# Kernel tuning notes

Hardware: AMD Instinct MI355X
Metric: run time of the kernel (lower is better)

## Reference

```python
import jax, jax.numpy as jnp
import numpy as np

H = 1024      # hidden_size
L = 2         # num_layers
B = 4096      # batch_size (acts as sequential time axis)
IN = 33       # LSTM input size (17 raw + 8 ip-embed + 8 port-embed)


def setup_inputs() -> dict:
    key = jax.random.key(0)
    ks = jax.random.split(key, 16)
    s = 0.02
    return {
        "x": jax.random.normal(ks[0], (B, 17), dtype=jnp.float32),
        "ip": jax.random.randint(ks[1], (B, 8), 0, 256),
        "port": jax.random.randint(ks[2], (B, 2), 0, 70000),
        "hidden": jnp.zeros((L, 1, H), dtype=jnp.float32),
        "cell": jnp.zeros((L, 1, H), dtype=jnp.float32),
        "ip_emb": jax.random.normal(ks[3], (256, 1), dtype=jnp.float32) * s,
        "port_emb": jax.random.normal(ks[4], (70000, 4), dtype=jnp.float32) * s,
        "W_ih0": jax.random.normal(ks[5], (4 * H, IN), dtype=jnp.float32) * s,
        "W_hh0": jax.random.normal(ks[6], (4 * H, H), dtype=jnp.float32) * s,
        "b_ih0": jax.random.normal(ks[7], (4 * H,), dtype=jnp.float32) * s,
        "b_hh0": jax.random.normal(ks[8], (4 * H,), dtype=jnp.float32) * s,
        "W_ih1": jax.random.normal(ks[9], (4 * H, H), dtype=jnp.float32) * s,
        "W_hh1": jax.random.normal(ks[10], (4 * H, H), dtype=jnp.float32) * s,
        "b_ih1": jax.random.normal(ks[11], (4 * H,), dtype=jnp.float32) * s,
        "b_hh1": jax.random.normal(ks[12], (4 * H,), dtype=jnp.float32) * s,
    }


def reference(x, ip, port, hidden, cell, ip_emb, port_emb,
              W_ih0, W_hh0, b_ih0, b_hh0, W_ih1, W_hh1, b_ih1, b_hh1):
    # embedding lookups + concat -> [B, 33]
    ip_e = ip_emb[ip].reshape(B, -1)        # [B, 8]
    port_e = port_emb[port].reshape(B, -1)  # [B, 8]
    xin = jnp.concatenate((x, ip_e, port_e), axis=1)  # [B, 33]

    Wih = (W_ih0, W_ih1)
    Whh = (W_hh0, W_hh1)
    bih = (b_ih0, b_ih1)
    bhh = (b_hh0, b_hh1)

    h0 = hidden[:, 0]  # [L, H]
    c0 = cell[:, 0]    # [L, H]

    def step(carry, xt):
        h, c = carry
        inp = xt
        hs, cs = [], []
        for l in range(L):  # fixed small layer loop
            gates = Wih[l] @ inp + bih[l] + Whh[l] @ h[l] + bhh[l]  # [4H]
            i, f, g, o = jnp.split(gates, 4)  # PyTorch gate order: i,f,g,o
            i = jax.nn.sigmoid(i)
            f = jax.nn.sigmoid(f)
            g = jnp.tanh(g)
            o = jax.nn.sigmoid(o)
            c_new = f * c[l] + i * g
            h_new = o * jnp.tanh(c_new)
            hs.append(h_new)
            cs.append(c_new)
            inp = h_new
        return (jnp.stack(hs), jnp.stack(cs)), jax.nn.relu(inp)

    (hf, cf), outputs = jax.lax.scan(step, (h0, c0), xin)
    return outputs, (hf[:, None, :], cf[:, None, :])
```

## Files before the change

kernel.cpp:

```cpp
#include <hip/hip_runtime.h>
#include <hip/hip_fp16.h>
#include <math.h>

#define Hn 1024
#define Bn 4096
#define INW 33
#define OUTS (Bn * Hn)
#define TPB 512
#define ROWP 1024

typedef _Float16 half2v __attribute__((ext_vector_type(2)));
typedef unsigned uint4v __attribute__((ext_vector_type(4)));

__device__ __forceinline__ float sigmoidf_(float x) {
    return 1.0f / (1.0f + __expf(-x));
}
__device__ __forceinline__ float tanhf_(float x) {
    float e = __expf(-2.0f * fabsf(x));
    float r = (1.0f - e) / (1.0f + e);
    return copysignf(r, x);
}
__device__ __forceinline__ unsigned pack2(float a, float b) {
    __half2 h = __floats2half2_rn(a, b);
    return __builtin_bit_cast(unsigned, h);
}
__device__ __forceinline__ float dot2acc(unsigned w, unsigned hv, float acc) {
#if __has_builtin(__builtin_amdgcn_fdot2)
    return __builtin_amdgcn_fdot2(__builtin_bit_cast(half2v, w),
                                  __builtin_bit_cast(half2v, hv), acc, false);
#else
    __half2 wh = __builtin_bit_cast(__half2, w);
    __half2 hh = __builtin_bit_cast(__half2, hv);
    float2 wf = __half22float2(wh), hf = __half22float2(hh);
    return acc + wf.x * hf.x + wf.y * hf.y;
#endif
}

__device__ __forceinline__ unsigned spin_slice(const unsigned long long* slice,
                                               int lane, unsigned tag) {
    unsigned long long v;
    int rounds = 0;
    for (;;) {
        asm volatile("global_load_dwordx2 %0, %1, off sc0 sc1\n\t"
                     "s_waitcnt vmcnt(0)"
                     : "=v"(v) : "v"(slice + lane) : "memory");
        if (__all((unsigned)(v >> 32) == tag)) break;
        if (++rounds > (1 << 24)) break;
    }
    return (unsigned)v;
}

__device__ __forceinline__ void spin_slice2(const unsigned long long* sliceA,
                                            const unsigned long long* sliceB,
                                            int lane, unsigned tag,
                                            unsigned& dA, unsigned& dB) {
    unsigned long long va, vb;
    int rounds = 0;
    for (;;) {
        asm volatile("global_load_dwordx2 %0, %2, off sc0 sc1\n\t"
                     "global_load_dwordx2 %1, %3, off sc0 sc1\n\t"
                     "s_waitcnt vmcnt(0)"
                     : "=v"(va), "=v"(vb)
                     : "v"(sliceA + lane), "v"(sliceB + lane) : "memory");
        bool ok = ((unsigned)(va >> 32) == tag) & ((unsigned)(vb >> 32) == tag);
        if (__all(ok)) break;
        if (++rounds > (1 << 24)) break;
    }
    dA = (unsigned)va;
    dB = (unsigned)vb;
}

__device__ __forceinline__ void store16_coherent(void* dst, uint4v v) {
    asm volatile("global_store_dwordx4 %0, %1, off sc0 sc1"
                 :: "v"(dst), "v"(v) : "memory");
}

__global__ void prep_kernel(const float* __restrict__ x, const int* __restrict__ ip,
                            const int* __restrict__ port, const float* __restrict__ ip_emb,
                            const float* __restrict__ port_emb, float* __restrict__ xin) {
    int gid = blockIdx.x * blockDim.x + threadIdx.x;
    if (gid < Bn * INW) {
        int t = gid / INW;
        int k = gid - t * INW;
        float v;
        if (k < 17) {
            v = x[t * 17 + k];
        } else if (k < 25) {
            v = ip_emb[ip[t * 8 + (k - 17)]];
        } else {
            int kk = k - 25;
            v = port_emb[port[t * 2 + (kk >> 2)] * 4 + (kk & 3)];
        }
        xin[gid] = v;
    }
}

__global__ void __launch_bounds__(TPB, 2) lstm_kernel(
    const float* __restrict__ xin,
    const float* __restrict__ hid0, const float* __restrict__ cel0,
    const float* __restrict__ Wih0, const float* __restrict__ Whh0,
    const float* __restrict__ bih0, const float* __restrict__ bhh0,
    const float* __restrict__ Wih1, const float* __restrict__ Whh1,
    const float* __restrict__ bih1, const float* __restrict__ bhh1,
    float* __restrict__ out,
    unsigned long long* __restrict__ rowpkt)
{
    __shared__ unsigned hs2[2][1024];
    __shared__ unsigned long long stg[16];
    const int tid  = threadIdx.x;
    const int lane = tid & 63;
    const int wave = tid >> 6;
    const int bx   = blockIdx.x;

    if (bx < 32) {
        const int j0 = bx * 32 + wave * 4;
        unsigned w2[4][4][8];
        float    wx[4][4];
        float    bs[4][4];
#pragma unroll
        for (int jj = 0; jj < 4; ++jj) {
#pragma unroll
            for (int g = 0; g < 4; ++g) {
                const int row = g * Hn + (j0 + jj);
                const float* wr = Whh0 + (size_t)row * Hn;
#pragma unroll
                for (int k = 0; k < 8; ++k) {
                    int c = lane + 64 * k;
                    w2[jj][g][k] = pack2(wr[2 * c], wr[2 * c + 1]);
                }
                wx[jj][g] = (lane < INW) ? Wih0[row * INW + lane] : 0.0f;
                bs[jj][g] = bih0[row] + bhh0[row];
            }
        }
        float cst[4], hcur[4];
#pragma unroll
        for (int jj = 0; jj < 4; ++jj) { cst[jj] = cel0[j0 + jj]; hcur[jj] = 0.0f; }

        for (int s = 0; s < Bn; ++s) {
            const int b = s & 1;
            float xv = xin[s * INW + (lane < INW ? lane : 0)];
            if (s == 0) {
                int q = wave * 64 + lane;
                hs2[0][q] = pack2(hid0[2 * q], hid0[2 * q + 1]);
            } else {
                unsigned d = spin_slice(rowpkt + (size_t)(s - 1) * ROWP + wave * 64,
                                        lane, (unsigned)s);
                hs2[b][wave * 64 + lane] = d;
            }
            __syncthreads();

            float acc[4][4];
#pragma unroll
            for (int jj = 0; jj < 4; ++jj)
#pragma unroll
                for (int g = 0; g < 4; ++g) acc[jj][g] = wx[jj][g] * xv;
#pragma unroll
            for (int k = 0; k < 8; ++k) {
                unsigned hv = hs2[b][lane + 64 * k];
#pragma unroll
                for (int jj = 0; jj < 4; ++jj)
#pragma unroll
                    for (int g = 0; g < 4; ++g)
                        acc[jj][g] = dot2acc(w2[jj][g][k], hv, acc[jj][g]);
            }

#pragma unroll
            for (int off = 32; off >= 1; off >>= 1)
#pragma unroll
                for (int jj = 0; jj < 4; ++jj)
#pragma unroll
                    for (int g = 0; g < 4; ++g)
                        acc[jj][g] += __shfl_xor(acc[jj][g], off);

#pragma unroll
            for (int jj = 0; jj < 4; ++jj) {
                float gi = sigmoidf_(acc[jj][0] + bs[jj][0]);
                float gf = sigmoidf_(acc[jj][1] + bs[jj][1]);
                float gg = tanhf_   (acc[jj][2] + bs[jj][2]);
                float go = sigmoidf_(acc[jj][3] + bs[jj][3]);
                cst[jj] = gf * cst[jj] + gi * gg;
                hcur[jj] = go * tanhf_(cst[jj]);
            }
            if (lane == 0) {
                unsigned long long tw = ((unsigned long long)(s + 1)) << 32;
                stg[2 * wave]     = tw | pack2(hcur[0], hcur[1]);
                stg[2 * wave + 1] = tw | pack2(hcur[2], hcur[3]);
            }
            __syncthreads();
            if (wave == 0 && lane < 8) {
                uint4v v = *(const uint4v*)&stg[2 * lane];
                char* dst = (char*)(rowpkt + (size_t)s * ROWP) + bx * 128 + lane * 16;
                store16_coherent(dst, v);
            }
        }
        if (lane == 0) {
#pragma unroll
            for (int jj = 0; jj < 4; ++jj) {
                out[OUTS + j0 + jj] = hcur[jj];
                out[OUTS + 2 * Hn + j0 + jj] = cst[jj];
            }
        }
    } else {
        const int blk = bx - 32;
        const int j0  = blk * 16 + wave * 2;
        unsigned w2[2][4][16];
        float    bs[2][4];
#pragma unroll
        for (int jj = 0; jj < 2; ++jj) {
#pragma unroll
            for (int g = 0; g < 4; ++g) {
                const int row = g * Hn + (j0 + jj);
                const float* wr1 = Wih1 + (size_t)row * Hn;
                const float* wr2 = Whh1 + (size_t)row * Hn;
#pragma unroll
                for (int k = 0; k < 8; ++k) {
                    int c = lane + 64 * k;
                    w2[jj][g][k]     = pack2(wr1[2 * c], wr1[2 * c + 1]);
                    w2[jj][g][8 + k] = pack2(wr2[2 * c], wr2[2 * c + 1]);
                }
                bs[jj][g] = bih1[row] + bhh1[row];
            }
        }
        float cst[2], hcur[2];
#pragma unroll
        for (int jj = 0; jj < 2; ++jj) { cst[jj] = cel0[Hn + j0 + jj]; hcur[jj] = 0.0f; }

        if (wave == 0 && lane < 4) {
            int base = Hn + blk * 16 + 4 * lane;
            uint4v v;
            v.x = pack2(hid0[base],     hid0[base + 1]);  v.y = 1u;
            v.z = pack2(hid0[base + 2], hid0[base + 3]);  v.w = 1u;
            char* dst = (char*)(rowpkt + 512) + blk * 64 + lane * 16;
            store16_coherent(dst, v);
        }

        for (int s = 1; s <= Bn; ++s) {
            const int t = s - 1;
            const int b = s & 1;
            const unsigned long long* rb = rowpkt + (size_t)(s - 1) * ROWP;
            unsigned dA, dB;
            spin_slice2(rb + wave * 64, rb + 512 + wave * 64, lane, (unsigned)s, dA, dB);
            hs2[b][wave * 64 + lane]       = dA;
            hs2[b][512 + wave * 64 + lane] = dB;
            __syncthreads();

            float acc[2][4];
#pragma unroll
            for (int jj = 0; jj < 2; ++jj)
#pragma unroll
                for (int g = 0; g < 4; ++g) acc[jj][g] = 0.0f;
#pragma unroll
            for (int k = 0; k < 16; ++k) {
                unsigned hv = hs2[b][lane + 64 * k];
#pragma unroll
                for (int jj = 0; jj < 2; ++jj)
#pragma unroll
                    for (int g = 0; g < 4; ++g)
                        acc[jj][g] = dot2acc(w2[jj][g][k], hv, acc[jj][g]);
            }

#pragma unroll
            for (int off = 32; off >= 1; off >>= 1)
#pragma unroll
                for (int jj = 0; jj < 2; ++jj)
#pragma unroll
                    for (int g = 0; g < 4; ++g)
                        acc[jj][g] += __shfl_xor(acc[jj][g], off);

#pragma unroll
            for (int jj = 0; jj < 2; ++jj) {
                float gi = sigmoidf_(acc[jj][0] + bs[jj][0]);
                float gf = sigmoidf_(acc[jj][1] + bs[jj][1]);
                float gg = tanhf_   (acc[jj][2] + bs[jj][2]);
                float go = sigmoidf_(acc[jj][3] + bs[jj][3]);
                cst[jj] = gf * cst[jj] + gi * gg;
                hcur[jj] = go * tanhf_(cst[jj]);
            }
            if (lane == 0) {
                unsigned long long tw = ((unsigned long long)(s + 1)) << 32;
                stg[wave] = tw | pack2(hcur[0], hcur[1]);
                float2 o2 = make_float2(fmaxf(hcur[0], 0.0f), fmaxf(hcur[1], 0.0f));
                *(float2*)(out + (size_t)t * Hn + j0) = o2;
            }
            __syncthreads();
            if (wave == 0 && lane < 4) {
                uint4v v = *(const uint4v*)&stg[2 * lane];
                char* dst = (char*)(rowpkt + (size_t)s * ROWP + 512) + blk * 64 + lane * 16;
                store16_coherent(dst, v);
            }
        }
        if (lane == 0) {
#pragma unroll
            for (int jj = 0; jj < 2; ++jj) {
                out[OUTS + Hn + j0 + jj] = hcur[jj];
                out[OUTS + 3 * Hn + j0 + jj] = cst[jj];
            }
        }
    }
}

extern "C" void kernel_launch(void* const* d_in, const int* in_sizes, int n_in,
                              void* d_out, int out_size, void* d_ws, size_t ws_size,
                              hipStream_t stream) {
    const float* x        = (const float*)d_in[0];
    const int*   ip       = (const int*)d_in[1];
    const int*   port     = (const int*)d_in[2];
    const float* hidden   = (const float*)d_in[3];
    const float* cell     = (const float*)d_in[4];
    const float* ip_emb   = (const float*)d_in[5];
    const float* port_emb = (const float*)d_in[6];
    const float* Wih0     = (const float*)d_in[7];
    const float* Whh0     = (const float*)d_in[8];
    const float* bih0     = (const float*)d_in[9];
    const float* bhh0     = (const float*)d_in[10];
    const float* Wih1     = (const float*)d_in[11];
    const float* Whh1     = (const float*)d_in[12];
    const float* bih1     = (const float*)d_in[13];
    const float* bhh1     = (const float*)d_in[14];
    float* out = (float*)d_out;

    unsigned long long* rowpkt = (unsigned long long*)d_ws;
    float* xin = (float*)(rowpkt + (size_t)(Bn + 1) * ROWP);

    prep_kernel<<<dim3((Bn * INW + 255) / 256), dim3(256), 0, stream>>>(
        x, ip, port, ip_emb, port_emb, xin);

    lstm_kernel<<<dim3(96), dim3(TPB), 0, stream>>>(
        xin, hidden, cell, Wih0, Whh0, bih0, bhh0, Wih1, Whh1, bih1, bhh1,
        out, rowpkt);
}
```

Measured before the change: 16.98 ms.

## Replace tagged-packet spin polling with per-step atomic counter flags

Inter-block hidden-state exchange changes from 64-bit packets carrying an inline step tag, which every lane polled, to a plain fp16 payload buffer plus per-step counters. Each producing block stores its data, waits for the stores, then atomically increments the flag. Consumers spin on a single flag word and then do one coherent load of the data. This halves the payload traffic and removes the wave-wide all-lanes tag check, at the cost of an extra atomic, a store-completion wait and a serial flag-then-data load latency per step. It also adds a memset of the flags before launch.

```diff
diff --git a/kernel.cpp b/kernel.cpp
--- a/kernel.cpp
+++ b/kernel.cpp
@@ -7,7 +7,9 @@
 #define INW 33
 #define OUTS (Bn * Hn)
 #define TPB 512
-#define ROWP 1024
+#define ROWU 1024
+#define FLAGSTRIDE 16
+#define BAILOUT (1 << 20)
 
 typedef _Float16 half2v __attribute__((ext_vector_type(2)));
 typedef unsigned uint4v __attribute__((ext_vector_type(4)));
@@ -36,43 +38,51 @@
 #endif
 }
 
-__device__ __forceinline__ unsigned spin_slice(const unsigned long long* slice,
-                                               int lane, unsigned tag) {
-    unsigned long long v;
+
+__device__ __forceinline__ void poll_flag32(const unsigned* fp, unsigned target) {
+    unsigned c;
+    int rounds = 0;
+    for (;;) {
+        asm volatile("global_load_dword %0, %1, off sc0 sc1\n\t"
+                     "s_waitcnt vmcnt(0)"
+                     : "=v"(c) : "v"(fp) : "memory");
+        if (c == target) break;
+        if (++rounds > BAILOUT) break;
+    }
+}
+__device__ __forceinline__ void poll_flag64(const unsigned long long* fp,
+                                            unsigned long long target) {
+    unsigned long long c;
     int rounds = 0;
     for (;;) {
         asm volatile("global_load_dwordx2 %0, %1, off sc0 sc1\n\t"
                      "s_waitcnt vmcnt(0)"
-                     : "=v"(v) : "v"(slice + lane) : "memory");
-        if (__all((unsigned)(v >> 32) == tag)) break;
-        if (++rounds > (1 << 24)) break;
+                     : "=v"(c) : "v"(fp) : "memory");
+        if (c == target) break;
+        if (++rounds > BAILOUT) break;
     }
-    return (unsigned)v;
-}
-
-__device__ __forceinline__ void spin_slice2(const unsigned long long* sliceA,
-                                            const unsigned long long* sliceB,
-                                            int lane, unsigned tag,
-                                            unsigned& dA, unsigned& dB) {
-    unsigned long long va, vb;
-    int rounds = 0;
-    for (;;) {
-        asm volatile("global_load_dwordx2 %0, %2, off sc0 sc1\n\t"
-                     "global_load_dwordx2 %1, %3, off sc0 sc1\n\t"
-                     "s_waitcnt vmcnt(0)"
-                     : "=v"(va), "=v"(vb)
-                     : "v"(sliceA + lane), "v"(sliceB + lane) : "memory");
-        bool ok = ((unsigned)(va >> 32) == tag) & ((unsigned)(vb >> 32) == tag);
-        if (__all(ok)) break;
-        if (++rounds > (1 << 24)) break;
-    }
-    dA = (unsigned)va;
-    dB = (unsigned)vb;
-}
-
+}
+
+__device__ __forceinline__ unsigned load4_coherent(const unsigned* p) {
+    unsigned d;
+    asm volatile("global_load_dword %0, %1, off sc0 sc1\n\t"
+                 "s_waitcnt vmcnt(0)"
+                 : "=v"(d) : "v"(p) : "memory");
+    return d;
+}
+__device__ __forceinline__ unsigned long long load8_coherent(const unsigned long long* p) {
+    unsigned long long d;
+    asm volatile("global_load_dwordx2 %0, %1, off sc0 sc1\n\t"
+                 "s_waitcnt vmcnt(0)"
+                 : "=v"(d) : "v"(p) : "memory");
+    return d;
+}
 __device__ __forceinline__ void store16_coherent(void* dst, uint4v v) {
     asm volatile("global_store_dwordx4 %0, %1, off sc0 sc1"
                  :: "v"(dst), "v"(v) : "memory");
+}
+__device__ __forceinline__ void wait_stores() {
+    asm volatile("s_waitcnt vmcnt(0)" ::: "memory");
 }
 
 __global__ void prep_kernel(const float* __restrict__ x, const int* __restrict__ ip,
@@ -103,10 +113,11 @@
     const float* __restrict__ Wih1, const float* __restrict__ Whh1,
     const float* __restrict__ bih1, const float* __restrict__ bhh1,
     float* __restrict__ out,
-    unsigned long long* __restrict__ rowpkt)
+    unsigned* __restrict__ hx,
+    unsigned* __restrict__ flags)
 {
     __shared__ unsigned hs2[2][1024];
-    __shared__ unsigned long long stg[16];
+    __shared__ unsigned stg[16];
     const int tid  = threadIdx.x;
     const int lane = tid & 63;
     const int wave = tid >> 6;
@@ -143,8 +154,8 @@
                 int q = wave * 64 + lane;
                 hs2[0][q] = pack2(hid0[2 * q], hid0[2 * q + 1]);
             } else {
-                unsigned d = spin_slice(rowpkt + (size_t)(s - 1) * ROWP + wave * 64,
-                                        lane, (unsigned)s);
+                poll_flag32(flags + (size_t)(s - 1) * FLAGSTRIDE, 32u);
+                unsigned d = load4_coherent(hx + (size_t)(s - 1) * ROWU + wave * 64 + lane);
                 hs2[b][wave * 64 + lane] = d;
             }
             __syncthreads();
@@ -182,15 +193,19 @@
                 hcur[jj] = go * tanhf_(cst[jj]);
             }
             if (lane == 0) {
-                unsigned long long tw = ((unsigned long long)(s + 1)) << 32;
-                stg[2 * wave]     = tw | pack2(hcur[0], hcur[1]);
-                stg[2 * wave + 1] = tw | pack2(hcur[2], hcur[3]);
+                stg[2 * wave]     = pack2(hcur[0], hcur[1]);
+                stg[2 * wave + 1] = pack2(hcur[2], hcur[3]);
             }
             __syncthreads();
-            if (wave == 0 && lane < 8) {
-                uint4v v = *(const uint4v*)&stg[2 * lane];
-                char* dst = (char*)(rowpkt + (size_t)s * ROWP) + bx * 128 + lane * 16;
-                store16_coherent(dst, v);
+            if (wave == 0) {
+                if (lane < 4) {
+                    uint4v v = *(const uint4v*)&stg[4 * lane];
+                    char* dst = (char*)(hx + (size_t)s * ROWU) + bx * 64 + lane * 16;
+                    store16_coherent(dst, v);
+                }
+                wait_stores();
+                if (lane == 0)
+                    atomicAdd(flags + (size_t)s * FLAGSTRIDE, 1u);
             }
         }
         if (lane == 0) {
@@ -225,23 +240,33 @@
 #pragma unroll
         for (int jj = 0; jj < 2; ++jj) { cst[jj] = cel0[Hn + j0 + jj]; hcur[jj] = 0.0f; }
 
-        if (wave == 0 && lane < 4) {
-            int base = Hn + blk * 16 + 4 * lane;
-            uint4v v;
-            v.x = pack2(hid0[base],     hid0[base + 1]);  v.y = 1u;
-            v.z = pack2(hid0[base + 2], hid0[base + 3]);  v.w = 1u;
-            char* dst = (char*)(rowpkt + 512) + blk * 64 + lane * 16;
-            store16_coherent(dst, v);
-        }
-
+        if (wave == 0) {
+            if (lane < 2) {
+                int base = Hn + blk * 16 + lane * 8;
+                uint4v v;
+                v.x = pack2(hid0[base],     hid0[base + 1]);
+                v.y = pack2(hid0[base + 2], hid0[base + 3]);
+                v.z = pack2(hid0[base + 4], hid0[base + 5]);
+                v.w = pack2(hid0[base + 6], hid0[base + 7]);
+                char* dst = (char*)(hx) + 2048 + blk * 32 + lane * 16;
+                store16_coherent(dst, v);
+            }
+            wait_stores();
+            if (lane == 0)
+                atomicAdd(flags + 1, 1u);
+        }
+
+        const unsigned long long target = 32ull | (64ull << 32);
         for (int s = 1; s <= Bn; ++s) {
             const int t = s - 1;
             const int b = s & 1;
-            const unsigned long long* rb = rowpkt + (size_t)(s - 1) * ROWP;
-            unsigned dA, dB;
-            spin_slice2(rb + wave * 64, rb + 512 + wave * 64, lane, (unsigned)s, dA, dB);
-            hs2[b][wave * 64 + lane]       = dA;
-            hs2[b][512 + wave * 64 + lane] = dB;
+            poll_flag64((const unsigned long long*)(flags + (size_t)(s - 1) * FLAGSTRIDE),
+                        target);
+            unsigned long long d = load8_coherent(
+                (const unsigned long long*)(hx + (size_t)(s - 1) * ROWU) + wave * 64 + lane);
+            int q = 2 * (wave * 64 + lane);
+            hs2[b][q]     = (unsigned)d;
+            hs2[b][q + 1] = (unsigned)(d >> 32);
             __syncthreads();
 
             float acc[2][4];
@@ -277,16 +302,20 @@
                 hcur[jj] = go * tanhf_(cst[jj]);
             }
             if (lane == 0) {
-                unsigned long long tw = ((unsigned long long)(s + 1)) << 32;
-                stg[wave] = tw | pack2(hcur[0], hcur[1]);
+                stg[wave] = pack2(hcur[0], hcur[1]);
                 float2 o2 = make_float2(fmaxf(hcur[0], 0.0f), fmaxf(hcur[1], 0.0f));
                 *(float2*)(out + (size_t)t * Hn + j0) = o2;
             }
             __syncthreads();
-            if (wave == 0 && lane < 4) {
-                uint4v v = *(const uint4v*)&stg[2 * lane];
-                char* dst = (char*)(rowpkt + (size_t)s * ROWP + 512) + blk * 64 + lane * 16;
-                store16_coherent(dst, v);
+            if (wave == 0) {
+                if (lane < 2) {
+                    uint4v v = *(const uint4v*)&stg[4 * lane];
+                    char* dst = (char*)(hx + (size_t)s * ROWU) + 2048 + blk * 32 + lane * 16;
+                    store16_coherent(dst, v);
+                }
+                wait_stores();
+                if (lane == 0)
+                    atomicAdd(flags + (size_t)s * FLAGSTRIDE + 1, 1u);
             }
         }
         if (lane == 0) {
@@ -319,13 +348,16 @@
     const float* bhh1     = (const float*)d_in[14];
     float* out = (float*)d_out;
 
-    unsigned long long* rowpkt = (unsigned long long*)d_ws;
-    float* xin = (float*)(rowpkt + (size_t)(Bn + 1) * ROWP);
+    unsigned* hx    = (unsigned*)d_ws;
+    unsigned* flags = hx + (size_t)(Bn + 1) * ROWU;
+    float*    xin   = (float*)(flags + (size_t)(Bn + 1) * FLAGSTRIDE);
+
+    hipMemsetAsync(flags, 0, (size_t)(Bn + 1) * FLAGSTRIDE * sizeof(unsigned), stream);
 
     prep_kernel<<<dim3((Bn * INW + 255) / 256), dim3(256), 0, stream>>>(
         x, ip, port, ip_emb, port_emb, xin);
 
     lstm_kernel<<<dim3(96), dim3(TPB), 0, stream>>>(
         xin, hidden, cell, Wih0, Whh0, bih0, bhh0, Wih1, Whh1, bih1, bhh1,
-        out, rowpkt);
-}
+        out, hx, flags);
+}
```

New measurement: 32.34 ms. 1.9x slower.
